# Performance work log

Measured on AMD Instinct MI355X. Metric: run time of the kernel, lower is better.

The kernel has to match this reference:

```python
import jax, jax.numpy as jnp
import numpy as np

NHEAD, DK, DV = 8, 32, 32
GRAPH = [[1,2,3,6,7],[1,2,4],[1,3,5],[2,4],[3,5],[1,6,8,12],[1,7,9,13],[6,8,10],[7,9,13],[8,10],[9,11],[9,12,14],[11,13,15],[12,14,16],[13,15,17],[14,16],[15,17]]
_idx = np.zeros((17,5), np.int32); _val = np.zeros((17,5), bool)
for _i, _nb in enumerate(GRAPH):
    for _j, _n in enumerate(_nb):
        _idx[_i,_j] = _n-1; _val[_i,_j] = True
NBR_IDX = jnp.asarray(_idx)            # (17,5) neighbor table (pad idx 0)
NBR_VALID = jnp.asarray(_val)          # (17,5) valid-neighbor mask
ATT_MASK = jnp.asarray(np.concatenate([_val, np.ones((17,2), bool)], 1))  # (17,7): 5 local + 2 global keys
INV_SQRT_DK = float(1.0/np.sqrt(DK))

def _ln_c(x, g, b, eps=1e-6):
    # LayerNorm over channel axis of (B,C,L)
    m = x.mean(1, keepdims=True)
    v = x.var(1, keepdims=True)
    return (x - m) * jax.lax.rsqrt(v + eps) * g[None,:,None] + b[None,:,None]

def _bn3(x, g, b, eps=1e-5):
    # BatchNorm1d (training batch stats) per channel over (B,L); x:(B,C,L)
    m = x.mean((0,2), keepdims=True)
    v = x.var((0,2), keepdims=True)
    return (x - m) * jax.lax.rsqrt(v + eps) * g[None,:,None] + b[None,:,None]

def _pos_ffn(x, w1, b1, w2, b2, g, b):
    # x:(B,C,L); Linear over C, relu, Linear back, residual, BatchNorm1d
    h = jax.nn.relu(jnp.einsum('bcl,hc->bhl', x, w1) + b1[None,:,None])
    y = jnp.einsum('bhl,ch->bcl', h, w2) + b2[None,:,None] + x
    return _bn3(y, g, b)

def _unfold(t):
    # t:(B,C,17) -> (B,C,5,17): per-node 5-wide neighbor window, zero padded
    g = t[:,:,NBR_IDX]                              # (B,C,17,5)
    g = jnp.where(NBR_VALID[None,None], g, 0.0)
    return jnp.transpose(g, (0,1,3,2))

def _sju(xn, ax, wq,bq,wk,bk,wv,bv, bng,bnb, f1w,f1b,f2w,f2b,fg,fb):
    B, C, L = xn.shape
    q = (jnp.einsum('oc,bcl->bol', wq, xn) + bq[None,:,None]).reshape(B,NHEAD,DK,L)
    kx = jnp.einsum('oc,bcl->bol', wk, xn) + bk[None,:,None]
    vx = jnp.einsum('oc,bcl->bol', wv, xn) + bv[None,:,None]
    k = _unfold(kx).reshape(B,NHEAD,DK,5,L)
    v = _unfold(vx).reshape(B,NHEAD,DV,5,L)
    ak = (jnp.einsum('oc,bcal->boal', wk, ax) + bk[None,:,None,None]).reshape(B,NHEAD,DK,2,L)
    av = (jnp.einsum('oc,bcal->boal', wv, ax) + bv[None,:,None,None]).reshape(B,NHEAD,DV,2,L)
    k = jnp.concatenate([k, ak], 3)                 # (B,H,dk,7,L)
    v = jnp.concatenate([v, av], 3)
    pre = jnp.einsum('bhdl,bhdwl->bhwl', q, k) * INV_SQRT_DK
    pre = jnp.where(ATT_MASK.T[None,None], pre, -jnp.inf)
    a = jax.nn.softmax(pre, axis=2)
    att = jnp.einsum('bhwl,bhdwl->bhdl', a, v).reshape(B,C,L)
    ret = _bn3(xn + att, bng, bnb)
    return _pos_ffn(ret, f1w,f1b,f2w,f2b,fg,fb)

def _sru(x, y, wq,bq,wk,bk,wv,bv, bng,bnb, f1w,f1b,f2w,f2b,fg,fb):
    # x:(B,C) relay, y:(B,C,Ly) keys/values
    B, C = x.shape
    q = (x @ wq.T + bq).reshape(B,NHEAD,DK)
    k = (jnp.einsum('oc,bcl->bol', wk, y) + bk[None,:,None]).reshape(B,NHEAD,DK,-1)
    v = (jnp.einsum('oc,bcl->bol', wv, y) + bv[None,:,None]).reshape(B,NHEAD,DV,-1)
    a = jax.nn.softmax(jnp.einsum('bhd,bhdl->bhl', q, k) * INV_SQRT_DK, axis=2)
    att = jnp.einsum('bhl,bhdl->bhd', a, v).reshape(B,C)
    ret = _bn3((x + att)[:,:,None], bng, bnb)
    return _pos_ffn(ret, f1w,f1b,f2w,f2b,fg,fb)[:,:,0]

def _forward(data, ln_g, ln_b, jq_w, jq_b, jk_w, jk_b, jv_w, jv_b, jbn_g, jbn_b, jf1_w, jf1_b, jf2_w, jf2_b, jfbn_g, jfbn_b, rq_w, rq_b, rk_w, rk_b, rv_w, rv_b, rbn_g, rbn_b, rf1_w, rf1_b, rf2_w, rf2_b, rfbn_g, rfbn_b):
    B, C, V, T = data.shape
    embs = jnp.transpose(data, (0,3,1,2)).reshape(B*T, C, V)   # fold time into batch
    nodes = embs
    relay = embs.mean(2)                                       # (BT,C)
    # ax: per node the 2 extra keys = its own original embedding + relay (fixed across layers)
    ax = jnp.stack([embs, jnp.broadcast_to(relay[:,:,None], embs.shape)], axis=2)  # (BT,C,2,V)
    for i in range(ln_g.shape[0]):
        xn = _ln_c(nodes, ln_g[i], ln_b[i])
        nodes = jax.nn.leaky_relu(_sju(xn, ax, jq_w[i],jq_b[i],jk_w[i],jk_b[i],jv_w[i],jv_b[i],jbn_g[i],jbn_b[i],jf1_w[i],jf1_b[i],jf2_w[i],jf2_b[i],jfbn_g[i],jfbn_b[i]), 0.01)
        y = jnp.concatenate([relay[:,:,None], nodes], axis=2)   # (BT,C,18)
        relay = jax.nn.leaky_relu(_sru(relay, y, rq_w[i],rq_b[i],rk_w[i],rk_b[i],rv_w[i],rv_b[i],rbn_g[i],rbn_b[i],rf1_w[i],rf1_b[i],rf2_w[i],rf2_b[i],rfbn_g[i],rfbn_b[i]), 0.01)
    return jnp.transpose(nodes.reshape(B,T,C,V), (0,2,3,1))

def setup_inputs():
    key = jax.random.key(0)
    Lyr, C, DIN, B, T, V = 2, 256, 1024, 4, 256, 17
    ks = jax.random.split(key, 40)
    ctr = [0]
    def nxt():
        k = ks[ctr[0]]; ctr[0] += 1; return k
    def w(shape, s=0.05):
        return jax.random.normal(nxt(), shape, jnp.float32) * s
    ones = lambda: jnp.ones((Lyr, C), jnp.float32)
    zeros = lambda: jnp.zeros((Lyr, C), jnp.float32)
    inp = {'data': jax.random.normal(nxt(), (B,C,V,T), jnp.float32),
           'ln_g': ones(), 'ln_b': zeros()}
    for p in ('j', 'r'):
        inp[p+'q_w'] = w((Lyr,C,C)); inp[p+'q_b'] = w((Lyr,C))
        inp[p+'k_w'] = w((Lyr,C,C)); inp[p+'k_b'] = w((Lyr,C))
        inp[p+'v_w'] = w((Lyr,C,C)); inp[p+'v_b'] = w((Lyr,C))
        inp[p+'bn_g'] = ones(); inp[p+'bn_b'] = zeros()
        inp[p+'f1_w'] = w((Lyr,DIN,C)); inp[p+'f1_b'] = w((Lyr,DIN))
        inp[p+'f2_w'] = w((Lyr,C,DIN)); inp[p+'f2_b'] = w((Lyr,C))
        inp[p+'fbn_g'] = ones(); inp[p+'fbn_b'] = zeros()
    return inp

def reference(data, ln_g, ln_b, jq_w, jq_b, jk_w, jk_b, jv_w, jv_b, jbn_g, jbn_b, jf1_w, jf1_b, jf2_w, jf2_b, jfbn_g, jfbn_b, rq_w, rq_b, rk_w, rk_b, rv_w, rv_b, rbn_g, rbn_b, rf1_w, rf1_b, rf2_w, rf2_b, rfbn_g, rfbn_b):
    return _forward(data, ln_g, ln_b, jq_w, jq_b, jk_w, jk_b, jv_w, jv_b, jbn_g, jbn_b, jf1_w, jf1_b, jf2_w, jf2_b, jfbn_g, jfbn_b, rq_w, rq_b, rk_w, rk_b, rv_w, rv_b, rbn_g, rbn_b, rf1_w, rf1_b, rf2_w, rf2_b, rfbn_g, rfbn_b)
```

## Files before the change

kernel.cpp:

```cpp
#include <hip/hip_runtime.h>
#include <hip/hip_bf16.h>


using bf16 = __hip_bfloat16;
typedef __attribute__((ext_vector_type(8))) short bf16x8v;
typedef __attribute__((ext_vector_type(4))) float f32x4;

namespace {
constexpr int kBT = 1024;
constexpr int kC = 256;
constexpr int kV = 17;
constexpr int kT = 256;
constexpr int kDIN = 1024;
constexpr int kRows = kBT * kV;
constexpr int kRowsE = kRows + kBT;
constexpr float kInvSqrtDk = 0.17677669529663687f;
constexpr size_t SZ_BIG = (size_t)kRows * kC;
}

__constant__ int c_nbi[17][5] = {
    {0, 1, 2, 5, 6},   {0, 1, 3, 0, 0},   {0, 2, 4, 0, 0},  {1, 3, 0, 0, 0},
    {2, 4, 0, 0, 0},   {0, 5, 7, 11, 0},  {0, 6, 8, 12, 0}, {5, 7, 9, 0, 0},
    {6, 8, 12, 0, 0},  {7, 9, 0, 0, 0},   {8, 10, 0, 0, 0}, {8, 11, 13, 0, 0},
    {10, 12, 14, 0, 0},{11, 13, 15, 0, 0},{12, 14, 16, 0, 0},
    {13, 15, 0, 0, 0}, {14, 16, 0, 0, 0}};
__constant__ int c_ncnt[17] = {5, 3, 3, 2, 2, 4, 4, 3, 3, 2, 2, 3, 3, 3, 3, 2, 2};

__device__ inline float bf2f(unsigned short s) {
  unsigned int u = ((unsigned int)s) << 16;
  float f;
  __builtin_memcpy(&f, &u, 4);
  return f;
}
__device__ inline unsigned short f2bf(float f) {
  unsigned int u;
  __builtin_memcpy(&u, &f, 4);
  unsigned int r = (u + 0x7fffu + ((u >> 16) & 1u)) >> 16;
  return (unsigned short)r;
}
__device__ inline float4 ldbf4(const bf16* p) {
  ushort4 u = *(const ushort4*)p;
  return make_float4(bf2f(u.x), bf2f(u.y), bf2f(u.z), bf2f(u.w));
}
__device__ inline void stbf4(bf16* p, float4 v) {
  ushort4 u = make_ushort4(f2bf(v.x), f2bf(v.y), f2bf(v.z), f2bf(v.w));
  *(ushort4*)p = u;
}
__device__ inline float dot4(float4 a, float4 b) {
  return a.x * b.x + a.y * b.y + a.z * b.z + a.w * b.w;
}

__device__ inline void async16(const bf16* g, bf16* l) {
  __builtin_amdgcn_global_load_lds(
      (const __attribute__((address_space(1))) void*)g,
      (__attribute__((address_space(3))) void*)l, 16, 0, 0);
}

template <int KT>
__global__ __launch_bounds__(256, 4) void k_mfma_gemm(
    const bf16* __restrict__ A, const bf16* __restrict__ W,
    const float* __restrict__ bias, const float* __restrict__ res,
    float* __restrict__ outF, bf16* __restrict__ outB,
    const float* __restrict__ bnScI, const float* __restrict__ bnShI,
    float* __restrict__ partOut, int nbPart, int N, int flags) {
  __shared__ __align__(16) char smem_raw[32768];
  bf16* As = (bf16*)smem_raw;
  bf16* Bs = (bf16*)(smem_raw + 16384);
  const int tid = threadIdx.x;
  const int wave = tid >> 6;
  const int lane = tid & 63;
  const int row0 = blockIdx.x * 128;
  const int col0 = blockIdx.y * 128;

  const int sub = lane >> 2;
  const int kq = (lane & 3) * 8;
  const int rg0 = (2 * wave + 0) * 16;
  const int rg1 = (2 * wave + 1) * 16;
  const bf16* ag0 = A + (size_t)(row0 + rg0 + sub) * KT + kq;
  const bf16* ag1 = A + (size_t)(row0 + rg1 + sub) * KT + kq;
  const bf16* bg0 = W + (size_t)(col0 + rg0 + sub) * KT + kq;
  const bf16* bg1 = W + (size_t)(col0 + rg1 + sub) * KT + kq;

  const int wm = wave >> 1, wn = wave & 1;
  const int fr = lane & 15;
  const int fk = (lane >> 4) * 8;

  f32x4 acc[4][4];
#pragma unroll
  for (int i = 0; i < 4; ++i)
#pragma unroll
    for (int j = 0; j < 4; ++j) acc[i][j] = (f32x4){0.f, 0.f, 0.f, 0.f};

#define STAGE32(buf, koff)                              \
  do {                                                  \
    async16(ag0 + (koff), As + (buf) * 4096 + rg0 * 32); \
    async16(ag1 + (koff), As + (buf) * 4096 + rg1 * 32); \
    async16(bg0 + (koff), Bs + (buf) * 4096 + rg0 * 32); \
    async16(bg1 + (koff), Bs + (buf) * 4096 + rg1 * 32); \
  } while (0)

  STAGE32(0, 0);
  __syncthreads();

  for (int k0 = 0; k0 < KT; k0 += 32) {
    const int cur = (k0 >> 5) & 1;
    if (k0 + 32 < KT) STAGE32(cur ^ 1, k0 + 32);
    bf16x8v af[4], bfv[4];
#pragma unroll
    for (int i = 0; i < 4; ++i)
      af[i] = *(const bf16x8v*)&As[cur * 4096 +
                                   (wm * 64 + i * 16 + fr) * 32 + fk];
#pragma unroll
    for (int j = 0; j < 4; ++j)
      bfv[j] = *(const bf16x8v*)&Bs[cur * 4096 +
                                    (wn * 64 + j * 16 + fr) * 32 + fk];
#pragma unroll
    for (int i = 0; i < 4; ++i)
#pragma unroll
      for (int j = 0; j < 4; ++j)
        acc[i][j] = __builtin_amdgcn_mfma_f32_16x16x32_bf16(af[i], bfv[j],
                                                            acc[i][j], 0, 0,
                                                            0);
    __syncthreads();
  }
#undef STAGE32

  if (flags & 4) {
    unsigned short* cs = (unsigned short*)smem_raw;
#pragma unroll
    for (int j = 0; j < 4; ++j) {
      int lc = wn * 64 + j * 16 + fr;
      float bv = bias ? bias[col0 + lc] : 0.f;
#pragma unroll
      for (int i = 0; i < 4; ++i) {
        int lr = wm * 64 + i * 16 + (lane >> 4) * 4;
#pragma unroll
        for (int r = 0; r < 4; ++r) {
          float v = acc[i][j][r] + bv;
          if (flags & 1) v = fmaxf(v, 0.f);
          cs[(lr + r) * 128 + lc] = f2bf(v);
        }
      }
    }
    __syncthreads();
#pragma unroll
    for (int p = 0; p < 8; ++p) {
      int lr = p * 16 + (tid >> 4);
      int lc = (tid & 15) * 8;
      *(bf16x8v*)&outB[(size_t)(row0 + lr) * N + col0 + lc] =
          *(const bf16x8v*)&cs[lr * 128 + lc];
    }
  } else {
    const int crow = row0 + wm * 64;
    const int ccol = col0 + wn * 64;
    float colS[4] = {0.f, 0.f, 0.f, 0.f};
    float colQ[4] = {0.f, 0.f, 0.f, 0.f};
#pragma unroll
    for (int j = 0; j < 4; ++j) {
      int col = ccol + j * 16 + fr;
      float bv = bias ? bias[col] : 0.f;
      float rsc = 1.f, rsh = 0.f;
      if (flags & 8) { rsc = bnScI[col]; rsh = bnShI[col]; }
#pragma unroll
      for (int i = 0; i < 4; ++i) {
        int rowb = crow + i * 16 + (lane >> 4) * 4;
#pragma unroll
        for (int r = 0; r < 4; ++r) {
          size_t row = (size_t)(rowb + r);
          float v = acc[i][j][r] + bv;
          if (res) v += res[row * N + col] * rsc + rsh;
          if (flags & 1) v = fmaxf(v, 0.f);
          outF[row * N + col] = v;
          colS[j] += v;
          colQ[j] += v * v;
        }
      }
    }
    if (flags & 8) {
#pragma unroll
      for (int j = 0; j < 4; ++j) {
        colS[j] += __shfl_xor(colS[j], 16);
        colS[j] += __shfl_xor(colS[j], 32);
        colQ[j] += __shfl_xor(colQ[j], 16);
        colQ[j] += __shfl_xor(colQ[j], 32);
      }
      float* sred = (float*)smem_raw;
      float* qred = sred + 4 * 64;
      if (lane < 16) {
#pragma unroll
        for (int j = 0; j < 4; ++j) {
          sred[wave * 64 + j * 16 + fr] = colS[j];
          qred[wave * 64 + j * 16 + fr] = colQ[j];
        }
      }
      __syncthreads();
      if (tid < 128) {
        int wn2 = tid >> 6, c = tid & 63;
        float s = sred[wn2 * 64 + c] + sred[(wn2 | 2) * 64 + c];
        float q = qred[wn2 * 64 + c] + qred[(wn2 | 2) * 64 + c];
        int col = col0 + wn2 * 64 + c;
        partOut[(size_t)blockIdx.x * kC + col] = s;
        partOut[(size_t)(nbPart + blockIdx.x) * kC + col] = q;
      }
    }
  }
}

__global__ __launch_bounds__(256) void k_xform_in(const float* __restrict__ data,
                                                  float* __restrict__ nodes,
                                                  bf16* __restrict__ embs_bf) {
  __shared__ float tile[32][33];
  int ct = blockIdx.x * 32, tt = blockIdx.y * 32;
  int bv = blockIdx.z;
  int b = bv / kV, v = bv - b * kV;
  int tx = threadIdx.x & 31, ty = threadIdx.x >> 5;
  for (int i = ty; i < 32; i += 8)
    tile[i][tx] = data[(((size_t)b * kC + ct + i) * kV + v) * kT + tt + tx];
  __syncthreads();
  for (int i = ty; i < 32; i += 8) {
    size_t s = (size_t)b * kT + tt + i;
    size_t idx = (s * kV + v) * kC + ct + tx;
    float val = tile[tx][i];
    nodes[idx] = val;
    embs_bf[idx] = __float2bfloat16(val);
  }
}

__global__ __launch_bounds__(256) void k_xform_out(const float* __restrict__ Z,
                                                   const float* __restrict__ scale,
                                                   const float* __restrict__ shift,
                                                   float* __restrict__ out) {
  __shared__ float tile[32][33];
  int ct = blockIdx.x * 32, tt = blockIdx.y * 32;
  int bv = blockIdx.z;
  int b = bv / kV, v = bv - b * kV;
  int tx = threadIdx.x & 31, ty = threadIdx.x >> 5;
  float sc = scale[ct + tx], sh = shift[ct + tx];
  for (int i = ty; i < 32; i += 8) {
    size_t s = (size_t)b * kT + tt + i;
    float val = Z[(s * kV + v) * kC + ct + tx] * sc + sh;
    val = (val > 0.f) ? val : 0.01f * val;
    tile[i][tx] = val;
  }
  __syncthreads();
  for (int i = ty; i < 32; i += 8)
    out[(((size_t)b * kC + ct + i) * kV + v) * kT + tt + tx] = tile[tx][i];
}

__global__ __launch_bounds__(256) void k_relay_init(const float* __restrict__ nodes,
                                                    bf16* __restrict__ relay0_bf) {
  int t = threadIdx.x;
  int s = blockIdx.x * 4 + (t >> 6);
  int c4 = (t & 63) * 4;
  float4 acc = make_float4(0.f, 0.f, 0.f, 0.f);
#pragma unroll
  for (int v = 0; v < kV; ++v) {
    float4 x = *(const float4*)(nodes + ((size_t)s * kV + v) * kC + c4);
    acc.x += x.x; acc.y += x.y; acc.z += x.z; acc.w += x.w;
  }
  float4 r = make_float4(acc.x / 17.f, acc.y / 17.f, acc.z / 17.f, acc.w / 17.f);
  stbf4(relay0_bf + (size_t)s * kC + c4, r);
}

__global__ __launch_bounds__(256) void k_layernorm(const float* __restrict__ X,
                                                   const float* __restrict__ g,
                                                   const float* __restrict__ b,
                                                   float* __restrict__ O,
                                                   bf16* __restrict__ Ob) {
  int t = threadIdx.x;
  int row = blockIdx.x * 4 + (t >> 6);
  int c4 = (t & 63) * 4;
  size_t i = (size_t)row * kC + c4;
  float4 x = *(const float4*)(X + i);
  float s = x.x + x.y + x.z + x.w;
  float q = dot4(x, x);
#pragma unroll
  for (int o = 32; o >= 1; o >>= 1) {
    s += __shfl_xor(s, o);
    q += __shfl_xor(q, o);
  }
  float m = s * (1.f / 256.f);
  float var = q * (1.f / 256.f) - m * m;
  float rs = rsqrtf(var + 1e-6f);
  float4 g4 = *(const float4*)(g + c4);
  float4 b4 = *(const float4*)(b + c4);
  float4 o4 = make_float4((x.x - m) * rs * g4.x + b4.x,
                          (x.y - m) * rs * g4.y + b4.y,
                          (x.z - m) * rs * g4.z + b4.z,
                          (x.w - m) * rs * g4.w + b4.w);
  *(float4*)(O + i) = o4;
  stbf4(Ob + i, o4);
}

__global__ __launch_bounds__(256) void k_attn_sat(const bf16* __restrict__ qkv,
                                                  const bf16* __restrict__ akav,
                                                  float* __restrict__ z,
                                                  float* __restrict__ part,
                                                  int nb) {
  __shared__ float sS[4][256];
  __shared__ float qS[4][256];
  int t = threadIdx.x;
  int w = t >> 6;
  int rl = blockIdx.x * 4 + w;
  int lane = t & 63;
  int s = rl / kV, l = rl - s * kV;
  int c4 = lane * 4;
  float4 q = ldbf4(qkv + (size_t)rl * 768 + c4);
  int cnt = c_ncnt[l];
  float sc[7];
  int nrow[5];
#pragma unroll
  for (int wd = 0; wd < 5; ++wd) {
    nrow[wd] = s * kV + c_nbi[l][wd];
    float4 k = ldbf4(qkv + (size_t)nrow[wd] * 768 + 256 + c4);
    float p = dot4(q, k);
    p += __shfl_xor(p, 1, 8);
    p += __shfl_xor(p, 2, 8);
    p += __shfl_xor(p, 4, 8);
    sc[wd] = (wd < cnt) ? p * kInvSqrtDk : -1e30f;
  }
  {
    float4 k = ldbf4(akav + (size_t)rl * 1024 + c4);
    float p = dot4(q, k);
    p += __shfl_xor(p, 1, 8);
    p += __shfl_xor(p, 2, 8);
    p += __shfl_xor(p, 4, 8);
    sc[5] = p * kInvSqrtDk;
  }
  {
    float4 k = ldbf4(akav + (size_t)(kRows + s) * 1024 + c4);
    float p = dot4(q, k);
    p += __shfl_xor(p, 1, 8);
    p += __shfl_xor(p, 2, 8);
    p += __shfl_xor(p, 4, 8);
    sc[6] = p * kInvSqrtDk;
  }
  float mx = sc[0];
#pragma unroll
  for (int wd = 1; wd < 7; ++wd) mx = fmaxf(mx, sc[wd]);
  float den = 0.f;
#pragma unroll
  for (int wd = 0; wd < 7; ++wd) {
    sc[wd] = __expf(sc[wd] - mx);
    den += sc[wd];
  }
  float inv = 1.f / den;
  float4 acc = make_float4(0.f, 0.f, 0.f, 0.f);
#pragma unroll
  for (int wd = 0; wd < 5; ++wd) {
    float4 v = ldbf4(qkv + (size_t)nrow[wd] * 768 + 512 + c4);
    acc.x += sc[wd] * v.x; acc.y += sc[wd] * v.y;
    acc.z += sc[wd] * v.z; acc.w += sc[wd] * v.w;
  }
  {
    float4 v = ldbf4(akav + (size_t)rl * 1024 + 256 + c4);
    acc.x += sc[5] * v.x; acc.y += sc[5] * v.y;
    acc.z += sc[5] * v.z; acc.w += sc[5] * v.w;
  }
  {
    float4 v = ldbf4(akav + (size_t)(kRows + s) * 1024 + 256 + c4);
    acc.x += sc[6] * v.x; acc.y += sc[6] * v.y;
    acc.z += sc[6] * v.z; acc.w += sc[6] * v.w;
  }
  size_t zi = (size_t)rl * kC + c4;
  float4 xv = *(const float4*)(z + zi);
  float4 o = make_float4(xv.x + acc.x * inv, xv.y + acc.y * inv,
                         xv.z + acc.z * inv, xv.w + acc.w * inv);
  *(float4*)(z + zi) = o;
  sS[w][c4 + 0] = o.x; sS[w][c4 + 1] = o.y;
  sS[w][c4 + 2] = o.z; sS[w][c4 + 3] = o.w;
  qS[w][c4 + 0] = o.x * o.x; qS[w][c4 + 1] = o.y * o.y;
  qS[w][c4 + 2] = o.z * o.z; qS[w][c4 + 3] = o.w * o.w;
  __syncthreads();
  float ps = sS[0][t] + sS[1][t] + sS[2][t] + sS[3][t];
  float pq = qS[0][t] + qS[1][t] + qS[2][t] + qS[3][t];
  part[(size_t)blockIdx.x * kC + t] = ps;
  part[(size_t)(nb + blockIdx.x) * kC + t] = pq;
}

__global__ __launch_bounds__(256) void k_bn_finalize(const float* __restrict__ part,
                                                     int nb, float inv_n,
                                                     const float* __restrict__ g,
                                                     const float* __restrict__ b,
                                                     float* __restrict__ scale,
                                                     float* __restrict__ shift) {
  int c = blockIdx.x;
  int t = threadIdx.x;
  float s = 0.f, q = 0.f;
  for (int i = t; i < nb; i += 256) {
    s += part[(size_t)i * kC + c];
    q += part[(size_t)(nb + i) * kC + c];
  }
#pragma unroll
  for (int o = 32; o >= 1; o >>= 1) {
    s += __shfl_xor(s, o);
    q += __shfl_xor(q, o);
  }
  __shared__ float ws[4], wq[4];
  int wid = t >> 6;
  if ((t & 63) == 0) { ws[wid] = s; wq[wid] = q; }
  __syncthreads();
  if (t == 0) {
    float S = ws[0] + ws[1] + ws[2] + ws[3];
    float Q = wq[0] + wq[1] + wq[2] + wq[3];
    float m = S * inv_n;
    float var = Q * inv_n - m * m;
    float sc = g[c] * rsqrtf(var + 1e-5f);
    scale[c] = sc;
    shift[c] = b[c] - m * sc;
  }
}

__global__ __launch_bounds__(256) void k_bn_apply(const float* __restrict__ Z,
                                                  const float* __restrict__ scale,
                                                  const float* __restrict__ shift,
                                                  float* __restrict__ outF,
                                                  bf16* __restrict__ outB,
                                                  int leaky) {
  int t = threadIdx.x;
  int row = blockIdx.x * 4 + (t >> 6);
  int c4 = (t & 63) * 4;
  size_t i = (size_t)row * kC + c4;
  float4 z = *(const float4*)(Z + i);
  float4 sc = *(const float4*)(scale + c4);
  float4 sh = *(const float4*)(shift + c4);
  float4 v = make_float4(z.x * sc.x + sh.x, z.y * sc.y + sh.y,
                         z.z * sc.z + sh.z, z.w * sc.w + sh.w);
  if (leaky) {
    v.x = (v.x > 0.f) ? v.x : 0.01f * v.x;
    v.y = (v.y > 0.f) ? v.y : 0.01f * v.y;
    v.z = (v.z > 0.f) ? v.z : 0.01f * v.z;
    v.w = (v.w > 0.f) ? v.w : 0.01f * v.w;
  }
  if (outF) *(float4*)(outF + i) = v;
  if (outB) stbf4(outB + i, v);
}

__global__ __launch_bounds__(256) void k_bn_ln(
    const float* __restrict__ Z, const float* __restrict__ scale,
    const float* __restrict__ shift, const float* __restrict__ g,
    const float* __restrict__ b, float* __restrict__ xnOut,
    bf16* __restrict__ actOut) {
  int t = threadIdx.x;
  int row = blockIdx.x * 4 + (t >> 6);
  int c4 = (t & 63) * 4;
  size_t i = (size_t)row * kC + c4;
  float4 z = *(const float4*)(Z + i);
  float4 sc = *(const float4*)(scale + c4);
  float4 sh = *(const float4*)(shift + c4);
  float4 v = make_float4(z.x * sc.x + sh.x, z.y * sc.y + sh.y,
                         z.z * sc.z + sh.z, z.w * sc.w + sh.w);
  v.x = (v.x > 0.f) ? v.x : 0.01f * v.x;
  v.y = (v.y > 0.f) ? v.y : 0.01f * v.y;
  v.z = (v.z > 0.f) ? v.z : 0.01f * v.z;
  v.w = (v.w > 0.f) ? v.w : 0.01f * v.w;
  float s = v.x + v.y + v.z + v.w;
  float q = dot4(v, v);
#pragma unroll
  for (int o = 32; o >= 1; o >>= 1) {
    s += __shfl_xor(s, o);
    q += __shfl_xor(q, o);
  }
  float m = s * (1.f / 256.f);
  float var = q * (1.f / 256.f) - m * m;
  float rs = rsqrtf(var + 1e-6f);
  float4 g4 = *(const float4*)(g + c4);
  float4 b4 = *(const float4*)(b + c4);
  float4 o4 = make_float4((v.x - m) * rs * g4.x + b4.x,
                          (v.y - m) * rs * g4.y + b4.y,
                          (v.z - m) * rs * g4.z + b4.z,
                          (v.w - m) * rs * g4.w + b4.w);
  *(float4*)(xnOut + i) = o4;
  stbf4(actOut + i, o4);
}

struct CvtTab {
  const float* src[12];
  bf16* dst[12];
  int n[12];
};
__global__ __launch_bounds__(256) void k_cvt_multi(CvtTab t) {
  int c = blockIdx.y;
  int i = (blockIdx.x * 256 + threadIdx.x) * 4;
  if (i >= t.n[c]) return;
  float4 v = *(const float4*)(t.src[c] + i);
  stbf4(t.dst[c] + i, v);
}

struct BiasTab {
  const float* src[10];
  float* dst[10];
};
__global__ __launch_bounds__(256) void k_bias_cat(BiasTab t) {
  t.dst[blockIdx.x][threadIdx.x] = t.src[blockIdx.x][threadIdx.x];
}

extern "C" void kernel_launch(void* const* d_in, const int* in_sizes, int n_in,
                              void* d_out, int out_size, void* d_ws, size_t ws_size,
                              hipStream_t stream) {
  const float* data = (const float*)d_in[0];
  const float* ln_g = (const float*)d_in[1];
  const float* ln_b = (const float*)d_in[2];
  const float* jq_w = (const float*)d_in[3];
  const float* jq_b = (const float*)d_in[4];
  const float* jk_w = (const float*)d_in[5];
  const float* jk_b = (const float*)d_in[6];
  const float* jv_w = (const float*)d_in[7];
  const float* jv_b = (const float*)d_in[8];
  const float* jbn_g = (const float*)d_in[9];
  const float* jbn_b = (const float*)d_in[10];
  const float* jf1_w = (const float*)d_in[11];
  const float* jf1_b = (const float*)d_in[12];
  const float* jf2_w = (const float*)d_in[13];
  const float* jf2_b = (const float*)d_in[14];
  const float* jfbn_g = (const float*)d_in[15];
  const float* jfbn_b = (const float*)d_in[16];
  float* out = (float*)d_out;

  float* f = (float*)d_ws;
  float* nodes = f;    f += SZ_BIG;
  float* xn = f;       f += SZ_BIG;
  float* part = f;     f += 2 * (kRows / 4) * kC;
  float* scale = f;    f += kC;
  float* shift = f;    f += kC;
  float* cb_jqkv = f;  f += 2 * 768;
  float* cb_kv4 = f;   f += 1024;

  bf16* bfa = (bf16*)f;
  bf16* act_bf = bfa;   bfa += SZ_BIG;
  bf16* embsX_bf = bfa; bfa += (size_t)kRowsE * kC;
  bf16* P = bfa;        bfa += (size_t)kRows * kDIN;
  bf16* akavBuf = bfa;  bfa += (size_t)kRowsE * 1024;
  bf16* Wjqkv = bfa;    bfa += 2 * 768 * 256;
  bf16* Wkv4 = bfa;     bfa += 1024 * 256;
  bf16* Wjf1 = bfa;     bfa += 2 * 1024 * 256;
  bf16* Wjf2 = bfa;     bfa += 2 * 256 * 1024;

  bf16* relay0_bf = embsX_bf + SZ_BIG;
  bf16* qkv_bf = P;
  bf16* h_bf = P;
  float* y2 = xn;

  auto gemm = [&](const bf16* A, const bf16* W, const float* bias,
                  const float* res, float* oF, bf16* oB, const float* bnScI,
                  const float* bnShI, float* partOut, int nbPart, int M, int N,
                  int K, int flags) {
    dim3 g(M / 128, N / 128);
    if (K == 256)
      k_mfma_gemm<256><<<g, 256, 0, stream>>>(A, W, bias, res, oF, oB, bnScI,
                                              bnShI, partOut, nbPart, N, flags);
    else
      k_mfma_gemm<1024><<<g, 256, 0, stream>>>(A, W, bias, res, oF, oB, bnScI,
                                               bnShI, partOut, nbPart, N,
                                               flags);
  };

  {
    CvtTab t;
    for (int i = 0; i < 2; ++i) {
      const size_t om = (size_t)i * kC * kC;
      const float* s3[3] = {jq_w + om, jk_w + om, jv_w + om};
      bf16* d3[3] = {Wjqkv + (size_t)i * 768 * 256,
                     Wjqkv + (size_t)i * 768 * 256 + 65536,
                     Wjqkv + (size_t)i * 768 * 256 + 131072};
      for (int j = 0; j < 3; ++j) {
        t.src[i * 3 + j] = s3[j];
        t.dst[i * 3 + j] = d3[j];
        t.n[i * 3 + j] = 65536;
      }
    }
    t.src[6] = jk_w;                 t.dst[6] = Wkv4;               t.n[6] = 65536;
    t.src[7] = jv_w;                 t.dst[7] = Wkv4 + 65536;       t.n[7] = 65536;
    t.src[8] = jk_w + (size_t)65536; t.dst[8] = Wkv4 + 131072;      t.n[8] = 65536;
    t.src[9] = jv_w + (size_t)65536; t.dst[9] = Wkv4 + 196608;      t.n[9] = 65536;
    t.src[10] = jf1_w; t.dst[10] = Wjf1; t.n[10] = 2 * 1024 * 256;
    t.src[11] = jf2_w; t.dst[11] = Wjf2; t.n[11] = 2 * 256 * 1024;
    k_cvt_multi<<<dim3(512, 12), 256, 0, stream>>>(t);
  }
  {
    BiasTab t;
    for (int i = 0; i < 2; ++i) {
      t.src[i * 3 + 0] = jq_b + (size_t)i * kC;
      t.src[i * 3 + 1] = jk_b + (size_t)i * kC;
      t.src[i * 3 + 2] = jv_b + (size_t)i * kC;
      t.dst[i * 3 + 0] = cb_jqkv + i * 768;
      t.dst[i * 3 + 1] = cb_jqkv + i * 768 + 256;
      t.dst[i * 3 + 2] = cb_jqkv + i * 768 + 512;
    }
    t.src[6] = jk_b;       t.dst[6] = cb_kv4;
    t.src[7] = jv_b;       t.dst[7] = cb_kv4 + 256;
    t.src[8] = jk_b + kC;  t.dst[8] = cb_kv4 + 512;
    t.src[9] = jv_b + kC;  t.dst[9] = cb_kv4 + 768;
    k_bias_cat<<<10, 256, 0, stream>>>(t);
  }

  k_xform_in<<<dim3(8, 8, 4 * kV), 256, 0, stream>>>(data, nodes, embsX_bf);
  k_relay_init<<<kBT / 4, 256, 0, stream>>>(nodes, relay0_bf);

  gemm(embsX_bf, Wkv4, cb_kv4, nullptr, nullptr, akavBuf, nullptr, nullptr,
       nullptr, 0, kRowsE, 1024, 256, 4);

  k_layernorm<<<kRows / 4, 256, 0, stream>>>(nodes, ln_g, ln_b, xn, act_bf);

  for (int i = 0; i < 2; ++i) {
    const size_t ob = (size_t)i * kC, ofb1 = (size_t)i * kDIN;
    const bf16* Wj = Wjqkv + (size_t)i * 768 * 256;
    const bf16* Wf1 = Wjf1 + (size_t)i * 1024 * 256;
    const bf16* Wf2 = Wjf2 + (size_t)i * 256 * 1024;
    const float* cbj = cb_jqkv + i * 768;
    const int nbA = kRows / 4;
    const int nbG = kRows / 128;

    gemm(act_bf, Wj, cbj, nullptr, nullptr, qkv_bf, nullptr, nullptr, nullptr,
         0, kRows, 768, 256, 4);
    k_attn_sat<<<kRows / 4, 256, 0, stream>>>(qkv_bf, akavBuf + (size_t)i * 512,
                                              xn, part, nbA);
    k_bn_finalize<<<kC, 256, 0, stream>>>(part, nbA, 1.f / kRows, jbn_g + ob,
                                          jbn_b + ob, scale, shift);
    k_bn_apply<<<kRows / 4, 256, 0, stream>>>(xn, scale, shift, nullptr,
                                              act_bf, 0);
    gemm(act_bf, Wf1, jf1_b + ofb1, nullptr, nullptr, h_bf, nullptr, nullptr,
         nullptr, 0, kRows, 1024, 256, 4 | 1);
    gemm(h_bf, Wf2, jf2_b + ob, xn, y2, nullptr, scale, shift, part, nbG,
         kRows, 256, 1024, 2 | 8);
    k_bn_finalize<<<kC, 256, 0, stream>>>(part, nbG, 1.f / kRows, jfbn_g + ob,
                                          jfbn_b + ob, scale, shift);
    if (i == 0) {
      k_bn_ln<<<kRows / 4, 256, 0, stream>>>(y2, scale, shift, ln_g + kC,
                                             ln_b + kC, xn, act_bf);
    }
  }

  k_xform_out<<<dim3(8, 8, 4 * kV), 256, 0, stream>>>(y2, scale, shift, out);
  (void)in_sizes; (void)n_in; (void)out_size; (void)ws_size;
}
```

Baseline: 431.8 us.

## Load GEMM MFMA fragments directly from global memory, drop LDS staging

```diff
diff --git a/kernel.cpp b/kernel.cpp
--- a/kernel.cpp
+++ b/kernel.cpp
@@ -50,70 +50,42 @@
   return a.x * b.x + a.y * b.y + a.z * b.z + a.w * b.w;
 }
 
-__device__ inline void async16(const bf16* g, bf16* l) {
-  __builtin_amdgcn_global_load_lds(
-      (const __attribute__((address_space(1))) void*)g,
-      (__attribute__((address_space(3))) void*)l, 16, 0, 0);
-}
-
 template <int KT>
-__global__ __launch_bounds__(256, 4) void k_mfma_gemm(
+__global__ __launch_bounds__(256, 3) void k_mfma_gemm(
     const bf16* __restrict__ A, const bf16* __restrict__ W,
     const float* __restrict__ bias, const float* __restrict__ res,
     float* __restrict__ outF, bf16* __restrict__ outB,
     const float* __restrict__ bnScI, const float* __restrict__ bnShI,
     float* __restrict__ partOut, int nbPart, int N, int flags) {
   __shared__ __align__(16) char smem_raw[32768];
-  bf16* As = (bf16*)smem_raw;
-  bf16* Bs = (bf16*)(smem_raw + 16384);
   const int tid = threadIdx.x;
   const int wave = tid >> 6;
   const int lane = tid & 63;
   const int row0 = blockIdx.x * 128;
   const int col0 = blockIdx.y * 128;
 
-  const int sub = lane >> 2;
-  const int kq = (lane & 3) * 8;
-  const int rg0 = (2 * wave + 0) * 16;
-  const int rg1 = (2 * wave + 1) * 16;
-  const bf16* ag0 = A + (size_t)(row0 + rg0 + sub) * KT + kq;
-  const bf16* ag1 = A + (size_t)(row0 + rg1 + sub) * KT + kq;
-  const bf16* bg0 = W + (size_t)(col0 + rg0 + sub) * KT + kq;
-  const bf16* bg1 = W + (size_t)(col0 + rg1 + sub) * KT + kq;
-
   const int wm = wave >> 1, wn = wave & 1;
   const int fr = lane & 15;
   const int fk = (lane >> 4) * 8;
 
+  const bf16* Abase = A + (size_t)(row0 + wm * 64 + fr) * KT + fk;
+  const bf16* Bbase = W + (size_t)(col0 + wn * 64 + fr) * KT + fk;
+
   f32x4 acc[4][4];
 #pragma unroll
   for (int i = 0; i < 4; ++i)
 #pragma unroll
     for (int j = 0; j < 4; ++j) acc[i][j] = (f32x4){0.f, 0.f, 0.f, 0.f};
 
-#define STAGE32(buf, koff)                              \
-  do {                                                  \
-    async16(ag0 + (koff), As + (buf) * 4096 + rg0 * 32); \
-    async16(ag1 + (koff), As + (buf) * 4096 + rg1 * 32); \
-    async16(bg0 + (koff), Bs + (buf) * 4096 + rg0 * 32); \
-    async16(bg1 + (koff), Bs + (buf) * 4096 + rg1 * 32); \
-  } while (0)
-
-  STAGE32(0, 0);
-  __syncthreads();
-
-  for (int k0 = 0; k0 < KT; k0 += 32) {
-    const int cur = (k0 >> 5) & 1;
-    if (k0 + 32 < KT) STAGE32(cur ^ 1, k0 + 32);
+#pragma unroll 4
+  for (int kc = 0; kc < KT / 32; ++kc) {
     bf16x8v af[4], bfv[4];
 #pragma unroll
     for (int i = 0; i < 4; ++i)
-      af[i] = *(const bf16x8v*)&As[cur * 4096 +
-                                   (wm * 64 + i * 16 + fr) * 32 + fk];
+      af[i] = *(const bf16x8v*)(Abase + (size_t)i * 16 * KT + kc * 32);
 #pragma unroll
     for (int j = 0; j < 4; ++j)
-      bfv[j] = *(const bf16x8v*)&Bs[cur * 4096 +
-                                    (wn * 64 + j * 16 + fr) * 32 + fk];
+      bfv[j] = *(const bf16x8v*)(Bbase + (size_t)j * 16 * KT + kc * 32);
 #pragma unroll
     for (int i = 0; i < 4; ++i)
 #pragma unroll
@@ -121,9 +93,7 @@
         acc[i][j] = __builtin_amdgcn_mfma_f32_16x16x32_bf16(af[i], bfv[j],
                                                             acc[i][j], 0, 0,
                                                             0);
-    __syncthreads();
-  }
-#undef STAGE32
+  }
 
   if (flags & 4) {
     unsigned short* cs = (unsigned short*)smem_raw;
```

After: 599.7 us. 1.39x slower.

## Add 64x64-tile GEMM for FFN down-projection and merge bias-copy into convert kernel

Applied to the files above, without the earlier changes.

```diff
diff --git a/kernel.cpp b/kernel.cpp
--- a/kernel.cpp
+++ b/kernel.cpp
@@ -153,8 +153,6 @@
   } else {
     const int crow = row0 + wm * 64;
     const int ccol = col0 + wn * 64;
-    float colS[4] = {0.f, 0.f, 0.f, 0.f};
-    float colQ[4] = {0.f, 0.f, 0.f, 0.f};
 #pragma unroll
     for (int j = 0; j < 4; ++j) {
       int col = ccol + j * 16 + fr;
@@ -171,38 +169,129 @@
           if (res) v += res[row * N + col] * rsc + rsh;
           if (flags & 1) v = fmaxf(v, 0.f);
           outF[row * N + col] = v;
-          colS[j] += v;
-          colQ[j] += v * v;
         }
       }
     }
-    if (flags & 8) {
-#pragma unroll
-      for (int j = 0; j < 4; ++j) {
-        colS[j] += __shfl_xor(colS[j], 16);
-        colS[j] += __shfl_xor(colS[j], 32);
-        colQ[j] += __shfl_xor(colQ[j], 16);
-        colQ[j] += __shfl_xor(colQ[j], 32);
+  }
+  (void)partOut; (void)nbPart;
+}
+
+__global__ __launch_bounds__(256, 4) void k_mfma_gemm64(
+    const bf16* __restrict__ A, const bf16* __restrict__ W,
+    const float* __restrict__ bias, const float* __restrict__ res,
+    float* __restrict__ outF, const float* __restrict__ bnScI,
+    const float* __restrict__ bnShI, float* __restrict__ partOut, int nbPart,
+    int N) {
+  constexpr int KT = 1024;
+  __shared__ __align__(16) bf16 As[2][4096];
+  __shared__ __align__(16) bf16 Bs[2][4096];
+  __shared__ float sred[4 * 64];
+  __shared__ float qred[4 * 64];
+  const int tid = threadIdx.x;
+  const int wave = tid >> 6;
+  const int lane = tid & 63;
+  const int row0 = blockIdx.x * 64;
+  const int col0 = blockIdx.y * 64;
+
+  const int srow = wave * 16 + (lane >> 2);
+  const int skq = (lane & 3) * 8;
+  const bf16* ag = A + (size_t)(row0 + srow) * KT + skq;
+  const bf16* bg = W + (size_t)(col0 + srow) * KT + skq;
+
+  const int wm = wave >> 1, wn = wave & 1;
+  const int fr = lane & 15;
+  const int fk = (lane >> 4) * 8;
+
+  f32x4 acc[2][2];
+#pragma unroll
+  for (int i = 0; i < 2; ++i)
+#pragma unroll
+    for (int j = 0; j < 2; ++j) acc[i][j] = (f32x4){0.f, 0.f, 0.f, 0.f};
+
+#define STAGE64x64(buf, koff)                                      \
+  do {                                                             \
+    _Pragma("unroll") for (int kc = 0; kc < 2; ++kc) {             \
+      async16(ag + (koff) + kc * 32,                               \
+              &As[(buf)][kc * 2048 + wave * 512]);                 \
+      async16(bg + (koff) + kc * 32,                               \
+              &Bs[(buf)][kc * 2048 + wave * 512]);                 \
+    }                                                              \
+  } while (0)
+
+  STAGE64x64(0, 0);
+  __syncthreads();
+
+  for (int k0 = 0; k0 < KT; k0 += 64) {
+    const int cur = (k0 >> 6) & 1;
+    if (k0 + 64 < KT) STAGE64x64(cur ^ 1, k0 + 64);
+#pragma unroll
+    for (int kc = 0; kc < 2; ++kc) {
+      bf16x8v af[2], bfv[2];
+#pragma unroll
+      for (int i = 0; i < 2; ++i)
+        af[i] = *(const bf16x8v*)&As[cur][kc * 2048 +
+                                          (wm * 32 + i * 16 + fr) * 32 + fk];
+#pragma unroll
+      for (int j = 0; j < 2; ++j)
+        bfv[j] = *(const bf16x8v*)&Bs[cur][kc * 2048 +
+                                           (wn * 32 + j * 16 + fr) * 32 + fk];
+#pragma unroll
+      for (int i = 0; i < 2; ++i)
+#pragma unroll
+        for (int j = 0; j < 2; ++j)
+          acc[i][j] = __builtin_amdgcn_mfma_f32_16x16x32_bf16(af[i], bfv[j],
+                                                              acc[i][j], 0, 0,
+                                                              0);
+    }
+    __syncthreads();
+  }
+#undef STAGE64x64
+
+  const int crow = row0 + wm * 32;
+  const int ccol = col0 + wn * 32;
+  float colS[2] = {0.f, 0.f};
+  float colQ[2] = {0.f, 0.f};
+#pragma unroll
+  for (int j = 0; j < 2; ++j) {
+    int col = ccol + j * 16 + fr;
+    float bv = bias[col];
+    float rsc = bnScI[col], rsh = bnShI[col];
+#pragma unroll
+    for (int i = 0; i < 2; ++i) {
+      int rowb = crow + i * 16 + (lane >> 4) * 4;
+#pragma unroll
+      for (int r = 0; r < 4; ++r) {
+        size_t row = (size_t)(rowb + r);
+        float v = acc[i][j][r] + bv + res[row * N + col] * rsc + rsh;
+        outF[row * N + col] = v;
+        colS[j] += v;
+        colQ[j] += v * v;
       }
-      float* sred = (float*)smem_raw;
-      float* qred = sred + 4 * 64;
-      if (lane < 16) {
-#pragma unroll
-        for (int j = 0; j < 4; ++j) {
-          sred[wave * 64 + j * 16 + fr] = colS[j];
-          qred[wave * 64 + j * 16 + fr] = colQ[j];
-        }
-      }
-      __syncthreads();
-      if (tid < 128) {
-        int wn2 = tid >> 6, c = tid & 63;
-        float s = sred[wn2 * 64 + c] + sred[(wn2 | 2) * 64 + c];
-        float q = qred[wn2 * 64 + c] + qred[(wn2 | 2) * 64 + c];
-        int col = col0 + wn2 * 64 + c;
-        partOut[(size_t)blockIdx.x * kC + col] = s;
-        partOut[(size_t)(nbPart + blockIdx.x) * kC + col] = q;
-      }
-    }
+    }
+  }
+#pragma unroll
+  for (int j = 0; j < 2; ++j) {
+    colS[j] += __shfl_xor(colS[j], 16);
+    colS[j] += __shfl_xor(colS[j], 32);
+    colQ[j] += __shfl_xor(colQ[j], 16);
+    colQ[j] += __shfl_xor(colQ[j], 32);
+  }
+  if (lane < 16) {
+#pragma unroll
+    for (int j = 0; j < 2; ++j) {
+      sred[wave * 64 + j * 16 + fr] = colS[j];
+      qred[wave * 64 + j * 16 + fr] = colQ[j];
+    }
+  }
+  __syncthreads();
+  if (tid < 64) {
+    int c = tid;
+    int wsel = c >> 5, off = c & 31;
+    float s = sred[wsel * 64 + off] + sred[(wsel + 2) * 64 + off];
+    float q = qred[wsel * 64 + off] + qred[(wsel + 2) * 64 + off];
+    int col = col0 + c;
+    partOut[(size_t)blockIdx.x * kC + col] = s;
+    partOut[(size_t)(nbPart + blockIdx.x) * kC + col] = q;
   }
 }
 
@@ -478,21 +567,19 @@
   const float* src[12];
   bf16* dst[12];
   int n[12];
+  const float* bsrc[10];
+  float* bdst[10];
 };
 __global__ __launch_bounds__(256) void k_cvt_multi(CvtTab t) {
   int c = blockIdx.y;
+  if (c == 12) {
+    if (blockIdx.x < 10) t.bdst[blockIdx.x][threadIdx.x] = t.bsrc[blockIdx.x][threadIdx.x];
+    return;
+  }
   int i = (blockIdx.x * 256 + threadIdx.x) * 4;
   if (i >= t.n[c]) return;
   float4 v = *(const float4*)(t.src[c] + i);
   stbf4(t.dst[c] + i, v);
-}
-
-struct BiasTab {
-  const float* src[10];
-  float* dst[10];
-};
-__global__ __launch_bounds__(256) void k_bias_cat(BiasTab t) {
-  t.dst[blockIdx.x][threadIdx.x] = t.src[blockIdx.x][threadIdx.x];
 }
 
 extern "C" void kernel_launch(void* const* d_in, const int* in_sizes, int n_in,
@@ -542,17 +629,16 @@
   float* y2 = xn;
 
   auto gemm = [&](const bf16* A, const bf16* W, const float* bias,
-                  const float* res, float* oF, bf16* oB, const float* bnScI,
-                  const float* bnShI, float* partOut, int nbPart, int M, int N,
-                  int K, int flags) {
+                  bf16* oB, int M, int N, int K, int flags) {
     dim3 g(M / 128, N / 128);
     if (K == 256)
-      k_mfma_gemm<256><<<g, 256, 0, stream>>>(A, W, bias, res, oF, oB, bnScI,
-                                              bnShI, partOut, nbPart, N, flags);
+      k_mfma_gemm<256><<<g, 256, 0, stream>>>(A, W, bias, nullptr, nullptr,
+                                              oB, nullptr, nullptr, nullptr, 0,
+                                              N, flags);
     else
-      k_mfma_gemm<1024><<<g, 256, 0, stream>>>(A, W, bias, res, oF, oB, bnScI,
-                                               bnShI, partOut, nbPart, N,
-                                               flags);
+      k_mfma_gemm<1024><<<g, 256, 0, stream>>>(A, W, bias, nullptr, nullptr,
+                                               oB, nullptr, nullptr, nullptr,
+                                               0, N, flags);
   };
 
   {
@@ -575,30 +661,25 @@
     t.src[9] = jv_w + (size_t)65536; t.dst[9] = Wkv4 + 196608;      t.n[9] = 65536;
     t.src[10] = jf1_w; t.dst[10] = Wjf1; t.n[10] = 2 * 1024 * 256;
     t.src[11] = jf2_w; t.dst[11] = Wjf2; t.n[11] = 2 * 256 * 1024;
-    k_cvt_multi<<<dim3(512, 12), 256, 0, stream>>>(t);
-  }
-  {
-    BiasTab t;
     for (int i = 0; i < 2; ++i) {
-      t.src[i * 3 + 0] = jq_b + (size_t)i * kC;
-      t.src[i * 3 + 1] = jk_b + (size_t)i * kC;
-      t.src[i * 3 + 2] = jv_b + (size_t)i * kC;
-      t.dst[i * 3 + 0] = cb_jqkv + i * 768;
-      t.dst[i * 3 + 1] = cb_jqkv + i * 768 + 256;
-      t.dst[i * 3 + 2] = cb_jqkv + i * 768 + 512;
-    }
-    t.src[6] = jk_b;       t.dst[6] = cb_kv4;
-    t.src[7] = jv_b;       t.dst[7] = cb_kv4 + 256;
-    t.src[8] = jk_b + kC;  t.dst[8] = cb_kv4 + 512;
-    t.src[9] = jv_b + kC;  t.dst[9] = cb_kv4 + 768;
-    k_bias_cat<<<10, 256, 0, stream>>>(t);
+      t.bsrc[i * 3 + 0] = jq_b + (size_t)i * kC;
+      t.bsrc[i * 3 + 1] = jk_b + (size_t)i * kC;
+      t.bsrc[i * 3 + 2] = jv_b + (size_t)i * kC;
+      t.bdst[i * 3 + 0] = cb_jqkv + i * 768;
+      t.bdst[i * 3 + 1] = cb_jqkv + i * 768 + 256;
+      t.bdst[i * 3 + 2] = cb_jqkv + i * 768 + 512;
+    }
+    t.bsrc[6] = jk_b;       t.bdst[6] = cb_kv4;
+    t.bsrc[7] = jv_b;       t.bdst[7] = cb_kv4 + 256;
+    t.bsrc[8] = jk_b + kC;  t.bdst[8] = cb_kv4 + 512;
+    t.bsrc[9] = jv_b + kC;  t.bdst[9] = cb_kv4 + 768;
+    k_cvt_multi<<<dim3(512, 13), 256, 0, stream>>>(t);
   }
 
   k_xform_in<<<dim3(8, 8, 4 * kV), 256, 0, stream>>>(data, nodes, embsX_bf);
   k_relay_init<<<kBT / 4, 256, 0, stream>>>(nodes, relay0_bf);
 
-  gemm(embsX_bf, Wkv4, cb_kv4, nullptr, nullptr, akavBuf, nullptr, nullptr,
-       nullptr, 0, kRowsE, 1024, 256, 4);
+  gemm(embsX_bf, Wkv4, cb_kv4, akavBuf, kRowsE, 1024, 256, 4);
 
   k_layernorm<<<kRows / 4, 256, 0, stream>>>(nodes, ln_g, ln_b, xn, act_bf);
 
@@ -609,20 +690,18 @@
     const bf16* Wf2 = Wjf2 + (size_t)i * 256 * 1024;
     const float* cbj = cb_jqkv + i * 768;
     const int nbA = kRows / 4;
-    const int nbG = kRows / 128;
-
-    gemm(act_bf, Wj, cbj, nullptr, nullptr, qkv_bf, nullptr, nullptr, nullptr,
-         0, kRows, 768, 256, 4);
+    const int nbG = kRows / 64;
+
+    gemm(act_bf, Wj, cbj, qkv_bf, kRows, 768, 256, 4);
     k_attn_sat<<<kRows / 4, 256, 0, stream>>>(qkv_bf, akavBuf + (size_t)i * 512,
                                               xn, part, nbA);
     k_bn_finalize<<<kC, 256, 0, stream>>>(part, nbA, 1.f / kRows, jbn_g + ob,
                                           jbn_b + ob, scale, shift);
     k_bn_apply<<<kRows / 4, 256, 0, stream>>>(xn, scale, shift, nullptr,
                                               act_bf, 0);
-    gemm(act_bf, Wf1, jf1_b + ofb1, nullptr, nullptr, h_bf, nullptr, nullptr,
-         nullptr, 0, kRows, 1024, 256, 4 | 1);
-    gemm(h_bf, Wf2, jf2_b + ob, xn, y2, nullptr, scale, shift, part, nbG,
-         kRows, 256, 1024, 2 | 8);
+    gemm(act_bf, Wf1, jf1_b + ofb1, h_bf, kRows, 1024, 256, 4 | 1);
+    k_mfma_gemm64<<<dim3(kRows / 64, kC / 64), 256, 0, stream>>>(
+        h_bf, Wf2, jf2_b + ob, xn, y2, scale, shift, part, nbG, kC);
     k_bn_finalize<<<kC, 256, 0, stream>>>(part, nbG, 1.f / kRows, jfbn_g + ob,
                                           jfbn_b + ob, scale, shift);
     if (i == 0) {
```

New measurement: 407.3 us (median of 2 runs). 1.06x faster.
